# Performance work log

Hardware: AMD Instinct MI355X
Metric: run time of the kernel (lower is better)

Reference implementation:

```python
import jax, jax.numpy as jnp
import numpy as np

DN = ('NCHW', 'OIHW', 'NCHW')

def conv(x, w, b, stride=1, pad=1):
    y = jax.lax.conv_general_dilated(x, w, (stride, stride), [(pad, pad), (pad, pad)], dimension_numbers=DN)
    return y + b[None, :, None, None]

def conv_t(x, w, b):
    # torch ConvTranspose2d(k=4, s=2, p=1): implemented as lhs-dilated conv, pad = k-1-p = 2
    y = jax.lax.conv_general_dilated(x, w, (1, 1), [(2, 2), (2, 2)], lhs_dilation=(2, 2), dimension_numbers=DN)
    return y + b[None, :, None, None]

def residual_stack(x, rw3, rb3, rw1, rb1):
    # canonical VQ-VAE residual block: x + conv1x1(relu(conv3x3(relu(x)))), then final relu
    n = rw3.shape[0]
    for i in range(n):
        h = conv(jax.nn.relu(x), rw3[i], rb3[i], 1, 1)
        h = conv(jax.nn.relu(h), rw1[i], rb1[i], 1, 0)
        x = x + h
    return jax.nn.relu(x)

def vq(x, codebook, beta):
    # x: [N, D, H, W] -> [N, H, W, D]
    x = jnp.transpose(x, (0, 2, 3, 1))
    shp = x.shape
    xf = x.reshape(-1, shp[-1])                               # [T, D]
    d = (jnp.sum(xf * xf, 1, keepdims=True)
         + jnp.sum(codebook * codebook, 1)
         - 2.0 * xf @ codebook.T)                             # [T, K]
    idx = jnp.argmin(d, axis=1)                               # [T]
    enc = jax.nn.one_hot(idx, codebook.shape[0], dtype=x.dtype)
    q = jnp.take(codebook, idx, axis=0).reshape(shp)
    loss_e = jnp.mean((jax.lax.stop_gradient(q) - x) ** 2)
    loss_q = jnp.mean((q - jax.lax.stop_gradient(x)) ** 2)
    loss = loss_q + beta * loss_e
    q_st = x + jax.lax.stop_gradient(q - x)
    p = jnp.mean(enc, axis=0)
    perplexity = jnp.exp(-jnp.sum(p * jnp.log(p + 1e-10)))
    return loss, jnp.transpose(q_st, (0, 3, 1, 2)), perplexity, enc

def setup_inputs() -> dict:
    key = jax.random.key(0)
    ks = jax.random.split(key, 24)
    C_img, C, RH, NR, K, D = 3, 128, 32, 2, 512, 64
    def g(k, shape, fan_in):
        return jax.random.normal(k, shape, jnp.float32) * (1.0 / np.sqrt(fan_in))
    inp = {
        'x': jax.random.normal(ks[0], (16, C_img, 256, 256), jnp.float32),
        'enc_w1': g(ks[1], (C // 2, C_img, 4, 4), C_img * 16), 'enc_b1': jnp.zeros((C // 2,)),
        'enc_w2': g(ks[2], (C, C // 2, 4, 4), C // 2 * 16), 'enc_b2': jnp.zeros((C,)),
        'enc_w3': g(ks[3], (C, C, 3, 3), C * 9), 'enc_b3': jnp.zeros((C,)),
        'enc_rw3': g(ks[4], (NR, RH, C, 3, 3), C * 9), 'enc_rb3': jnp.zeros((NR, RH)),
        'enc_rw1': g(ks[5], (NR, C, RH, 1, 1), RH), 'enc_rb1': jnp.zeros((NR, C)),
        'pre_w': g(ks[6], (D, C, 1, 1), C), 'pre_b': jnp.zeros((D,)),
        'codebook': jax.random.uniform(ks[7], (K, D), jnp.float32, -1.0 / K, 1.0 / K),
        'dec_w1': g(ks[8], (C, D, 3, 3), D * 9), 'dec_b1': jnp.zeros((C,)),
        'dec_rw3': g(ks[9], (NR, RH, C, 3, 3), C * 9), 'dec_rb3': jnp.zeros((NR, RH)),
        'dec_rw1': g(ks[10], (NR, C, RH, 1, 1), RH), 'dec_rb1': jnp.zeros((NR, C)),
        'dec_dw1': g(ks[11], (C // 2, C, 4, 4), C * 16), 'dec_db1': jnp.zeros((C // 2,)),
        'dec_dw2': g(ks[12], (C_img, C // 2, 4, 4), C // 2 * 16), 'dec_db2': jnp.zeros((C_img,)),
    }
    return inp

def reference(x, enc_w1, enc_b1, enc_w2, enc_b2, enc_w3, enc_b3, enc_rw3, enc_rb3, enc_rw1, enc_rb1,
              pre_w, pre_b, codebook, dec_w1, dec_b1, dec_rw3, dec_rb3, dec_rw1, dec_rb1,
              dec_dw1, dec_db1, dec_dw2, dec_db2):
    beta = 0.25
    # encoder
    h = jax.nn.relu(conv(x, enc_w1, enc_b1, 2, 1))
    h = jax.nn.relu(conv(h, enc_w2, enc_b2, 2, 1))
    h = conv(h, enc_w3, enc_b3, 1, 1)
    h = residual_stack(h, enc_rw3, enc_rb3, enc_rw1, enc_rb1)
    # pre-VQ 1x1 conv
    z = conv(h, pre_w, pre_b, 1, 0)
    # vector quantization
    loss, q, perplexity, _ = vq(z, codebook, beta)
    # decoder
    d = conv(q, dec_w1, dec_b1, 1, 1)
    d = residual_stack(d, dec_rw3, dec_rb3, dec_rw1, dec_rb1)
    d = jax.nn.relu(conv_t(d, dec_dw1, dec_db1))
    x_recon = conv_t(d, dec_dw2, dec_db2)
    return loss, x_recon, perplexity
```

## Files before the change

### kernel.cpp

```cpp
#include <hip/hip_runtime.h>

typedef __attribute__((ext_vector_type(8)))  short bf16x8;
typedef __attribute__((ext_vector_type(16))) float f32x16;
typedef unsigned long long u64t;

__device__ __forceinline__ int swzu(int u)
{
    return u ^ (((u >> 3) & 1) | (((u >> 4) & 1) << 1));
}

__device__ __forceinline__ void fsplit(float v, unsigned short& h, unsigned short& l)
{
    union { float f; unsigned u; } a; a.f = v;
    unsigned uh = a.u + 0x7fffu + ((a.u >> 16) & 1u);
    h = (unsigned short)(uh >> 16);
    union { float f; unsigned u; } hb; hb.u = (unsigned)h << 16;
    float r = v - hb.f;
    union { float f; unsigned u; } b; b.f = r;
    unsigned ul = b.u + 0x7fffu + ((b.u >> 16) & 1u);
    l = (unsigned short)(ul >> 16);
}

__device__ __forceinline__ float bf2f(unsigned short u)
{
    union { float f; unsigned v; } a; a.v = (unsigned)u << 16; return a.f;
}

__global__ void pack_w(const float* __restrict__ w, unsigned short* __restrict__ hi,
                       unsigned short* __restrict__ lo, int Cout, int Cin, int KK,
                       int CoP, int CiP)
{
    int i = blockIdx.x * 256 + threadIdx.x;
    int tot = KK * CoP * CiP;
    if (i >= tot) return;
    int t  = i / (CoP * CiP);
    int r  = i - t * (CoP * CiP);
    int co = r / CiP;
    int ci = r - co * CiP;
    float v = (co < Cout && ci < Cin) ? w[((size_t)co * Cin + ci) * KK + t] : 0.f;
    unsigned short h, l;
    fsplit(v, h, l);
    hi[i] = h; lo[i] = l;
}

__global__ void cb_norm(const float* __restrict__ cb, float* __restrict__ cn)
{
    int i = blockIdx.x * 256 + threadIdx.x;
    if (i >= 512) return;
    float s = 0.f;
    for (int d = 0; d < 64; d++) s = fmaf(cb[i*64+d], cb[i*64+d], s);
    cn[i] = s;
}

__global__ __launch_bounds__(256) void pack_x(const float* __restrict__ x,
    unsigned short* __restrict__ PH)
{
    int idx = blockIdx.x * 256 + threadIdx.x;
    int n = idx >> 16, pix = idx & 65535;
    unsigned short h[8], l[8];
#pragma unroll
    for (int c = 0; c < 8; c++) h[c] = 0;
#pragma unroll
    for (int c = 0; c < 3; c++) {
        float v = x[((size_t)(n * 3 + c) << 16) + pix];
        fsplit(v, h[c], l[c]);
    }
    uint4 hv;
    hv.x = h[0] | ((unsigned)h[1] << 16); hv.y = h[2] | ((unsigned)h[3] << 16);
    hv.z = h[4] | ((unsigned)h[5] << 16); hv.w = h[6] | ((unsigned)h[7] << 16);
    uint4 z4 = make_uint4(0, 0, 0, 0);
    size_t b0 = (((size_t)(n * 2) << 16) + pix) * 8;
    size_t b1 = (((size_t)(n * 2 + 1) << 16) + pix) * 8;
    *(uint4*)(PH + b0) = hv;
    *(uint4*)(PH + b1) = z4;
}

template<int K,int S,int P,int CIP,int COUT,int HIN,int WIN,int HOUT,int WOUT,
         int TR,int TC,int WM,int WN,int PX2,int CO2,int CC,int CO_PAD,
         bool PACK,bool PRELU,bool PLO,bool WF32,bool ROUT,bool RES>
__global__ __launch_bounds__(256) void conv_mfma(
    const unsigned short* __restrict__ inH,
    const unsigned short* __restrict__ wpH,
    const float* __restrict__ bias, const float* __restrict__ res,
    float* __restrict__ outF, unsigned short* __restrict__ outPH,
    unsigned short* __restrict__ outPL)
{
    constexpr int IHT = (TR - 1) * S + K;
    constexpr int IW  = (TC - 1) * S + K;
    constexpr int PS  = IHT * IW;
    constexpr int PLN = CC * 2;
    constexpr int UN  = PS * PLN;
    constexpr int KK  = K * K;
    constexpr int NCH = CIP / (CC * 16);
    constexpr int NBUF = (NCH > 1) ? 2 : 1;
    constexpr int CG  = CIP / 8;
    constexpr int CGO = (COUT + 7) / 8;
    constexpr int XB  = WOUT / TC;
    constexpr int REGU = (UN + 255) / 256;
    constexpr int NST = CC * KK;

    __shared__ uint4 lbH[NBUF * UN];

    const int tid = threadIdx.x;
    const int bx  = blockIdx.x;
    const int r0  = (bx / XB) * TR;
    const int c0  = (bx % XB) * TC;
    const int co0 = blockIdx.y * (WM * CO2 * 32);
    const int n   = blockIdx.z;

    const int l  = tid & 63, wv = tid >> 6;
    const int wm = wv / WN, wn = wv % WN;
    const int ln = l & 31, kg = l >> 5;

    int pb[PX2], gyv[PX2], gxv[PX2];
#pragma unroll
    for (int p2 = 0; p2 < PX2; p2++) {
        int q = wn * (PX2 * 32) + p2 * 32 + ln;
        int lr = q / TC, lc = q % TC;
        pb[p2] = (lr * S) * IW + lc * S;
        gyv[p2] = r0 + lr; gxv[p2] = c0 + lc;
    }

    const int iy0 = r0 * S - P, ix0 = c0 * S - P;
    const size_t inb = (size_t)n * CG * HIN * WIN;

    f32x16 acc[PX2][CO2];
#pragma unroll
    for (int p2 = 0; p2 < PX2; p2++)
#pragma unroll
        for (int g = 0; g < CO2; g++) acc[p2][g] = (f32x16){};

    auto unit_load = [&](int u, int cgb, uint4& hv){
        int kgu = u / PS, pos = u - kgu * PS;
        int py = pos / IW, px = pos - py * IW;
        int gy = iy0 + py, gx = ix0 + px;
        bool ok = ((unsigned)gy < (unsigned)HIN) && ((unsigned)gx < (unsigned)WIN);
        hv = make_uint4(0,0,0,0);
        if (ok) {
            size_t a = (inb + ((size_t)(cgb + kgu) * HIN + gy) * WIN + gx) * 8;
            hv = *(const uint4*)(inH + a);
        }
    };

    auto stage_direct = [&](int kc, int b){
        for (int idx = tid; idx < UN; idx += 256) {
            uint4 hv;
            unit_load(idx, kc * PLN, hv);
            lbH[b * UN + swzu(idx)] = hv;
        }
    };

    uint4 rvH[REGU];
    auto load_regs = [&](int kc){
#pragma unroll
        for (int rr = 0; rr < REGU; rr++) {
            int idx = tid + rr * 256;
            uint4 hv = make_uint4(0,0,0,0);
            if (idx < UN) unit_load(idx, kc * PLN, hv);
            rvH[rr] = hv;
        }
    };
    auto write_regs = [&](int b){
#pragma unroll
        for (int rr = 0; rr < REGU; rr++) {
            int idx = tid + rr * 256;
            if (idx < UN) lbH[b * UN + swzu(idx)] = rvH[rr];
        }
    };

    auto compute = [&](int kc, int b){
        bf16x8 aR[3][CO2], bR[2][PX2];
        auto loadA = [&](int step, bf16x8 (&a)[CO2]){
            const int ks = step / KK, t = step - ks * KK;
#pragma unroll
            for (int g = 0; g < CO2; g++) {
                const int coA = co0 + (wm * CO2 + g) * 32 + ln;
                const size_t wo = ((size_t)t * CO_PAD + coA) * CIP
                                + kc * (CC * 16) + ks * 16 + kg * 8;
                a[g] = *(const bf16x8*)(wpH + wo);
            }
        };
        auto loadB = [&](int step, bf16x8 (&bv)[PX2]){
            const int ks = step / KK, t = step - ks * KK;
            const int ky = t / K, kx = t - ky * K;
#pragma unroll
            for (int p2 = 0; p2 < PX2; p2++) {
                const int u = (ks * 2 + kg) * PS + pb[p2] + ky * IW + kx;
                bv[p2] = *(const bf16x8*)&lbH[b * UN + swzu(u)];
            }
        };
        loadA(0, aR[0]);
        if (NST > 1) loadA(1, aR[1]);
        loadB(0, bR[0]);
#pragma unroll
        for (int step = 0; step < NST; step++) {
            if (step + 2 < NST) loadA(step + 2, aR[(step + 2) % 3]);
            if (step + 1 < NST) loadB(step + 1, bR[(step + 1) & 1]);
#pragma unroll
            for (int p2 = 0; p2 < PX2; p2++)
#pragma unroll
                for (int g = 0; g < CO2; g++)
                    acc[p2][g] = __builtin_amdgcn_mfma_f32_32x32x16_bf16(
                        aR[step % 3][g], bR[step & 1][p2], acc[p2][g], 0, 0, 0);
        }
    };

    stage_direct(0, 0);
    __syncthreads();
    int cur = 0;
    for (int kc = 0; kc < NCH; kc++) {
        const bool more = (kc + 1 < NCH);
        if (more) load_regs(kc + 1);
        compute(kc, cur);
        if (more) {
            write_regs(cur ^ 1);
            __syncthreads();
            cur ^= 1;
        }
    }

    const size_t HWo = (size_t)HOUT * WOUT;
#pragma unroll
    for (int p2 = 0; p2 < PX2; p2++) {
        const int gy = gyv[p2], gx = gxv[p2];
#pragma unroll
        for (int g = 0; g < CO2; g++) {
            const int co32 = co0 + (wm * CO2 + g) * 32;
#pragma unroll
            for (int rq = 0; rq < 4; rq++) {
                const int cb4 = co32 + 8 * rq + 4 * kg;
                float v[4];
#pragma unroll
                for (int i = 0; i < 4; i++) {
                    const int r = rq * 4 + i;
                    const int co = cb4 + i;
                    float bv = (co < COUT) ? bias[co] : 0.f;
                    float vv = acc[p2][g][r] + bv;
                    if (RES && co < COUT)
                        vv += res[((size_t)n * COUT + co) * HWo + (size_t)gy * WOUT + gx];
                    if (ROUT) vv = fmaxf(vv, 0.f);
                    if (WF32 && co < COUT)
                        outF[((size_t)n * COUT + co) * HWo + (size_t)gy * WOUT + gx] = vv;
                    v[i] = vv;
                }
                if (PACK) {
                    u64t uh = 0, ul = 0;
#pragma unroll
                    for (int i = 0; i < 4; i++) {
                        float pv = PRELU ? fmaxf(v[i], 0.f) : v[i];
                        unsigned short ph, pl;
                        fsplit(pv, ph, pl);
                        uh |= (u64t)ph << (16 * i);
                        ul |= (u64t)pl << (16 * i);
                    }
                    size_t pa = (((size_t)n * CGO + (co32 >> 3) + rq) * HOUT + gy) * (size_t)WOUT * 8
                              + (size_t)gx * 8 + 4 * kg;
                    *(u64t*)(outPH + pa) = uh;
                    if (PLO) *(u64t*)(outPL + pa) = ul;
                }
            }
// ... 41 lines not shown
        float v[4];
#pragma unroll
        for (int i = 0; i < 4; i++) {
            const int r = rq * 4 + i;
            const int co = cb4 + i;
            float bv = (co < COUT) ? bias[co] : 0.f;
            float vv = acc[r] + bv;
            if (RES && co < COUT)
                vv += res[((size_t)n * COUT + co) * HW + pix];
            if (ROUT) vv = fmaxf(vv, 0.f);
            if (WF32 && co < COUT)
                outF[((size_t)n * COUT + co) * HW + pix] = vv;
            v[i] = vv;
        }
        if (PACK) {
            u64t uh = 0, ul = 0;
#pragma unroll
            for (int i = 0; i < 4; i++) {
                float pv = PRELU ? fmaxf(v[i], 0.f) : v[i];
                unsigned short ph, pl;
                fsplit(pv, ph, pl);
                uh |= (u64t)ph << (16 * i);
                ul |= (u64t)pl << (16 * i);
            }
            size_t pa = (((size_t)n * CGO + (co32 >> 3) + rq) * HW + pix) * 8 + 4 * kg;
            *(u64t*)(outPH + pa) = uh;
            if (PLO) *(u64t*)(outPL + pa) = ul;
        }
    }
}

template<int CIP,int COUT,int HIN,int WIN,int CO2,int CC,int CO_PAD,
         bool PACK,bool WF32,bool ROUT>
__global__ __launch_bounds__(256) void convt_mfma(
    const unsigned short* __restrict__ inH,
    const unsigned short* __restrict__ wpH,
    const float* __restrict__ bias, float* __restrict__ outF,
    unsigned short* __restrict__ outPH)
{
    constexpr int HOUT = 2 * HIN, WOUT = 2 * WIN;
    constexpr int XHN  = WOUT / 128;
    constexpr int PS   = 3 * 68;
    constexpr int PLN  = CC * 2;
    constexpr int UN   = PS * PLN;
    constexpr int NCH  = CIP / (CC * 16);
    constexpr int NBUF = (NCH > 1) ? 2 : 1;
    constexpr int CG   = CIP / 8;
    constexpr int CGO  = (COUT + 7) / 8;
    constexpr int REGU = (UN + 255) / 256;
    constexpr int NST  = CC * 4;

    __shared__ uint4 lbH[NBUF * UN];

    const int tid = threadIdx.x;
    const int xh  = blockIdx.x % XHN;
    const int gr  = blockIdx.x / XHN;
    const int oy0 = (gr >> 1) * 4 + (gr & 1);
    const int co0 = blockIdx.y * (CO2 * 32);
    const int n   = blockIdx.z;

    const int ky0 = oy0 & 1;
    const int iyb = ((oy0 + ky0) >> 1) - 1;

    const int l  = tid & 63, wv = tid >> 6;
    const int pw = wv & 1, xb = wv >> 1;
    const int ln = l & 31, kg = l >> 5;

    const size_t inb = (size_t)n * CG * HIN * WIN;

    f32x16 acc[2][CO2];
#pragma unroll
    for (int r2 = 0; r2 < 2; r2++)
#pragma unroll
        for (int g = 0; g < CO2; g++) acc[r2][g] = (f32x16){};

    auto unit_load = [&](int u, int cgb, uint4& hv){
        int kgu = u / PS, pos = u - kgu * PS;
        int rr = pos / 68, cc = pos - rr * 68;
        int gy = iyb + rr, gx = xh * 64 + cc - 1;
        bool ok = ((unsigned)gy < (unsigned)HIN) && ((unsigned)gx < (unsigned)WIN);
        hv = make_uint4(0,0,0,0);
        if (ok) {
            size_t a = (inb + ((size_t)(cgb + kgu) * HIN + gy) * WIN + gx) * 8;
            hv = *(const uint4*)(inH + a);
        }
    };

    auto stage_direct = [&](int kc, int b){
        for (int idx = tid; idx < UN; idx += 256) {
            uint4 hv;
            unit_load(idx, kc * PLN, hv);
            lbH[b * UN + swzu(idx)] = hv;
        }
    };

    uint4 rvH[REGU];
    auto load_regs = [&](int kc){
#pragma unroll
        for (int rr = 0; rr < REGU; rr++) {
            int idx = tid + rr * 256;
            uint4 hv = make_uint4(0,0,0,0);
            if (idx < UN) unit_load(idx, kc * PLN, hv);
            rvH[rr] = hv;
        }
    };
    auto write_regs = [&](int b){
#pragma unroll
        for (int rr = 0; rr < REGU; rr++) {
            int idx = tid + rr * 256;
            if (idx < UN) lbH[b * UN + swzu(idx)] = rvH[rr];
        }
    };

    auto compute = [&](int kc, int b){
        bf16x8 aR[3][CO2], bR[2][2];
        auto loadA = [&](int step, bf16x8 (&a)[CO2]){
            const int ks = step / 4, tt = step - ks * 4;
            const int widx = (ky0 + 2 * (tt >> 1)) * 4 + (pw + 2 * (tt & 1));
#pragma unroll
            for (int g = 0; g < CO2; g++) {
                const int coA = co0 + g * 32 + ln;
                const size_t wo = ((size_t)widx * CO_PAD + coA) * CIP
                                + kc * (CC * 16) + ks * 16 + kg * 8;
                a[g] = *(const bf16x8*)(wpH + wo);
            }
        };
        auto loadB = [&](int step, bf16x8 (&bv)[2]){
            const int ks = step / 4, tt = step - ks * 4;
            const int ty = tt >> 1, tx = tt & 1;
#pragma unroll
            for (int r2 = 0; r2 < 2; r2++) {
                const int u = (ks * 2 + kg) * PS + (r2 + ty) * 68 + xb * 32 + ln + pw + tx;
                bv[r2] = *(const bf16x8*)&lbH[b * UN + swzu(u)];
            }
        };
        loadA(0, aR[0]);
        if (NST > 1) loadA(1, aR[1]);
        loadB(0, bR[0]);
#pragma unroll
        for (int step = 0; step < NST; step++) {
            if (step + 2 < NST) loadA(step + 2, aR[(step + 2) % 3]);
            if (step + 1 < NST) loadB(step + 1, bR[(step + 1) & 1]);
#pragma unroll
            for (int r2 = 0; r2 < 2; r2++)
#pragma unroll
                for (int g = 0; g < CO2; g++)
                    acc[r2][g] = __builtin_amdgcn_mfma_f32_32x32x16_bf16(
                        aR[step % 3][g], bR[step & 1][r2], acc[r2][g], 0, 0, 0);
        }
    };

    stage_direct(0, 0);
    __syncthreads();
    int cur = 0;
    for (int kc = 0; kc < NCH; kc++) {
        const bool more = (kc + 1 < NCH);
        if (more) load_regs(kc + 1);
        compute(kc, cur);
        if (more) {
            write_regs(cur ^ 1);
            __syncthreads();
            cur ^= 1;
        }
    }

    const int ox = xh * 128 + pw + 2 * (xb * 32 + ln);
    const size_t HWo = (size_t)HOUT * WOUT;
#pragma unroll
    for (int r2 = 0; r2 < 2; r2++) {
        const int oy = oy0 + 2 * r2;
#pragma unroll
        for (int g = 0; g < CO2; g++) {
            const int co32 = co0 + g * 32;
#pragma unroll
            for (int rq = 0; rq < 4; rq++) {
                const int cb4 = co32 + 8 * rq + 4 * kg;
                float v[4];
#pragma unroll
                for (int i = 0; i < 4; i++) {
                    const int r = rq * 4 + i;
                    const int co = cb4 + i;
                    float bv = (co < COUT) ? bias[co] : 0.f;
                    float vv = acc[r2][g][r] + bv;
                    if (ROUT) vv = fmaxf(vv, 0.f);
                    if (WF32 && co < COUT)
                        outF[((size_t)n * COUT + co) * HWo + (size_t)oy * WOUT + ox] = vv;
                    v[i] = vv;
                }
                if (PACK) {
                    u64t uh = 0;
#pragma unroll
                    for (int i = 0; i < 4; i++) {
                        unsigned short ph, pl;
                        fsplit(v[i], ph, pl);
                        uh |= (u64t)ph << (16 * i);
                    }
                    size_t pa = (((size_t)n * CGO + (co32 >> 3) + rq) * HOUT + oy) * (size_t)WOUT * 8
                              + (size_t)ox * 8 + 4 * kg;
                    *(u64t*)(outPH + pa) = uh;
                }
            }
        }
    }
}

__global__ __launch_bounds__(256) void vq_mfma(
    const unsigned short* __restrict__ zPH, const unsigned short* __restrict__ zPL,
    const unsigned short* __restrict__ cbH, const unsigned short* __restrict__ cbL,
    const float* __restrict__ cnorm,
    unsigned short* __restrict__ qPH,
    float* __restrict__ ssep, int* __restrict__ hist)
{
    __shared__ unsigned short zH[128 * 72];
    __shared__ unsigned short zL[128 * 72];
    __shared__ float cnl[512];
    __shared__ int   hl[512];

    const int tid = threadIdx.x;
    const int blk = blockIdx.x;

    for (int i = tid; i < 512; i += 256) { cnl[i] = cnorm[i]; hl[i] = 0; }

    for (int idx = tid; idx < 1024; idx += 256) {
        int tok = idx >> 3, cg = idx & 7;
        int t = blk * 128 + tok;
        int n = t >> 12, pix = t & 4095;
        size_t a = (((size_t)(n * 8 + cg)) * 4096 + pix) * 8;
        *(uint4*)&zH[tok * 72 + cg * 8] = *(const uint4*)(zPH + a);
        *(uint4*)&zL[tok * 72 + cg * 8] = *(const uint4*)(zPL + a);
    }
    __syncthreads();

    const int l  = tid & 63, wv = tid >> 6;
// ... 30 lines not shown
        for (int r = 0; r < 16; r++) {
            int m    = (r & 3) + 8 * (r >> 2) + 4 * kg;
            int code = cg * 32 + m;
            float s  = a0[r] + a1[r];
            float dm = cnl[code] - 2.f * s;
            if (dm < bm) { bm = dm; bidx = code; }
        }
    }

    float bm2 = __shfl_xor(bm, 32);
    int   bi2 = __shfl_xor(bidx, 32);
    if (bm2 < bm || (bm2 == bm && bi2 < bidx)) { bm = bm2; bidx = bi2; }

    {
        int t = blk * 128 + tok;
        int n = t >> 12, pix = t & 4095;
#pragma unroll
        for (int cgl = 0; cgl < 4; cgl++) {
            int cg = kg * 4 + cgl;
            uint4 hv = *(const uint4*)(cbH + (size_t)bidx * 64 + cg * 8);
            size_t a = (((size_t)(n * 8 + cg)) * 4096 + pix) * 8;
            *(uint4*)(qPH + a) = hv;
        }
    }

    float bestd = xn + bm;
    float c = (kg == 0) ? bestd : 0.f;
#pragma unroll
    for (int o = 32; o > 0; o >>= 1) c += __shfl_down(c, o, 64);
    if (l == 0) ssep[blk * 4 + wv] = c;
    if (kg == 0) atomicAdd(&hl[bidx], 1);
    __syncthreads();
    for (int i = tid; i < 512; i += 256) if (hl[i] > 0) atomicAdd(&hist[i], hl[i]);
}

__global__ void vq_init(int* hist)
{
    for (int i = threadIdx.x; i < 512; i += 256) hist[i] = 0;
}

__global__ __launch_bounds__(256) void vq_finalize(
    const float* __restrict__ ssep, const int* __restrict__ hist,
    float* __restrict__ o_loss, float* __restrict__ o_perp)
{
    __shared__ float red[256];
    const int tid = threadIdx.x;
    float h = 0.f;
    for (int i = tid; i < 512; i += 256) {
        float p = (float)hist[i] * (1.0f / 65536.0f);
        h -= p * logf(p + 1e-10f);
    }
    red[tid] = h;
    __syncthreads();
    for (int st = 128; st > 0; st >>= 1) {
        if (tid < st) red[tid] += red[tid + st];
        __syncthreads();
    }
    const float H = red[0];
    __syncthreads();
    float s = 0.f;
    for (int i = tid; i < 2048; i += 256) s += ssep[i];
    red[tid] = s;
    __syncthreads();
    for (int st = 128; st > 0; st >>= 1) {
        if (tid < st) red[tid] += red[tid + st];
        __syncthreads();
    }
    if (tid == 0) {
        *o_loss = 1.25f * red[0] / 4194304.0f;
        *o_perp = expf(H);
    }
// ... 26 lines not shown
    const float* dw1     = (const float*)d_in[20];
    const float* db1     = (const float*)d_in[21];
    const float* dw2     = (const float*)d_in[22];
    const float* db2     = (const float*)d_in[23];

    float* o      = (float*)d_out;
    float* loss_p = o;
    float* recon  = o + 1;
    float* perp_p = o + 1 + 16 * 3 * 256 * 256;

    unsigned short* R1H = (unsigned short*)d_ws;
    unsigned short* R1L = R1H + 16777216;
    unsigned short* R2H = R1L + 16777216;
    unsigned short* R2L = R2H + 16777216;
    float* Cf  = (float*)(R2L + 16777216);
    float* SSE = Cf + 8388608;
    int*   HIST = (int*)(SSE + 2048);

    unsigned short *xPH = R1H;
    unsigned short *BPH = R1H;
    unsigned short *zPH = R1H + 8388608, *zPL = R1L + 8388608;
    unsigned short *DtPH = R1H + 12582912;
    unsigned short *dAPH = R1H;
    unsigned short *APH = R2H;
    unsigned short *CPH = R2H;
    unsigned short *qPH = R2H + 8388608;

    unsigned short* wp_cur = (unsigned short*)(((size_t)(HIST + 512) + 31) & ~(size_t)31);
    auto carve = [&](size_t n_us) {
        unsigned short* p = wp_cur;
        wp_cur += ((n_us + 15) & ~(size_t)15);
        return p;
    };
    auto PK = [&](const float* w, unsigned short* hi, unsigned short* lo,
                  int Co, int Ci, int KK, int CoP, int CiP) {
        int tot = KK * CoP * CiP;
        pack_w<<<dim3((tot + 255) / 256), dim3(256), 0, stream>>>(w, hi, lo, Co, Ci, KK, CoP, CiP);
    };

    unsigned short *e1H = carve(16*64*16),  *e1L = carve(16*64*16);
    unsigned short *e2H = carve(16*128*64), *e2L = carve(16*128*64);
    unsigned short *e3H = carve(9*128*128), *e3L = carve(9*128*128);
    unsigned short *er3aH = carve(9*32*128), *er3aL = carve(9*32*128);
    unsigned short *er3bH = carve(9*32*128), *er3bL = carve(9*32*128);
    unsigned short *er1aH = carve(128*32),   *er1aL = carve(128*32);
    unsigned short *er1bH = carve(128*32),   *er1bL = carve(128*32);
    unsigned short *preH = carve(64*128),    *preL = carve(64*128);
    unsigned short *d1H  = carve(9*128*64),  *d1L  = carve(9*128*64);
    unsigned short *dr3aH = carve(9*32*128), *dr3aL = carve(9*32*128);
    unsigned short *dr3bH = carve(9*32*128), *dr3bL = carve(9*32*128);
    unsigned short *dr1aH = carve(128*32),   *dr1aL = carve(128*32);
    unsigned short *dr1bH = carve(128*32),   *dr1bL = carve(128*32);
    unsigned short *ct1H = carve(16*64*128), *ct1L = carve(16*64*128);
    unsigned short *ct2H = carve(16*32*64),  *ct2L = carve(16*32*64);
    unsigned short *cbH  = carve(512*64),    *cbL  = carve(512*64);
    float* CN = (float*)carve(1024);

    PK(enc_w1, e1H, e1L, 64, 3, 16, 64, 16);
    PK(enc_w2, e2H, e2L, 128, 64, 16, 128, 64);
    PK(enc_w3, e3H, e3L, 128, 128, 9, 128, 128);
    PK(enc_rw3,             er3aH, er3aL, 32, 128, 9, 32, 128);
    PK(enc_rw3 + 32*128*9,  er3bH, er3bL, 32, 128, 9, 32, 128);
    PK(enc_rw1,             er1aH, er1aL, 128, 32, 1, 128, 32);
    PK(enc_rw1 + 128*32,    er1bH, er1bL, 128, 32, 1, 128, 32);
    PK(pre_w, preH, preL, 64, 128, 1, 64, 128);
    PK(dec_w1, d1H, d1L, 128, 64, 9, 128, 64);
    PK(dec_rw3,             dr3aH, dr3aL, 32, 128, 9, 32, 128);
    PK(dec_rw3 + 32*128*9,  dr3bH, dr3bL, 32, 128, 9, 32, 128);
    PK(dec_rw1,             dr1aH, dr1aL, 128, 32, 1, 128, 32);
    PK(dec_rw1 + 128*32,    dr1bH, dr1bL, 128, 32, 1, 128, 32);
    PK(dw1, ct1H, ct1L, 64, 128, 16, 64, 128);
    PK(dw2, ct2H, ct2L, 3, 64, 16, 32, 64);
    PK(cb,  cbH,  cbL,  512, 64, 1, 512, 64);
    cb_norm<<<dim3(2), dim3(256), 0, stream>>>(cb, CN);
    pack_x<<<dim3(4096), dim3(256), 0, stream>>>(x, xPH);

    const int N = 16;

    conv_mfma<4,2,1, 16,64, 256,256, 128,128, 1,64, 2,2,1,1, 1, 64,
              true,false,false,false,true,false>
        <<<dim3(256,1,N),256,0,stream>>>(xPH, e1H, enc_b1, nullptr, nullptr, APH, nullptr);
    conv_mfma<4,2,1, 64,128, 128,128, 64,64, 1,64, 4,1,2,1, 1, 128,
              true,false,false,false,true,false>
        <<<dim3(64,1,N),256,0,stream>>>(APH, e2H, enc_b2, nullptr, nullptr, BPH, nullptr);
    conv_mfma<3,1,1, 128,128, 64,64, 64,64, 1,64, 4,1,2,1, 2, 128,
              true,true,false,true,false,false>
        <<<dim3(64,1,N),256,0,stream>>>(BPH, e3H, enc_b3, nullptr, Cf, CPH, nullptr);
    conv_mfma<3,1,1, 128,32, 64,64, 64,64, 2,64, 1,4,1,1, 4, 32,
              true,true,false,false,false,false>
        <<<dim3(32,1,N),256,0,stream>>>(CPH, er3aH, enc_rb3, nullptr, nullptr, DtPH, nullptr);
    conv1x1_mfma<32,128, 4096, 128,  true,true,false,true,false,true>
        <<<dim3(64,2,N),256,0,stream>>>(DtPH, er1aH, enc_rb1, Cf, Cf, CPH, nullptr);
    conv_mfma<3,1,1, 128,32, 64,64, 64,64, 2,64, 1,4,1,1, 4, 32,
              true,true,false,false,false,false>
        <<<dim3(32,1,N),256,0,stream>>>(CPH, er3bH, enc_rb3 + 32, nullptr, nullptr, DtPH, nullptr);
    conv1x1_mfma<32,128, 4096, 128,  true,true,false,true,false,true>
        <<<dim3(64,2,N),256,0,stream>>>(DtPH, er1bH, enc_rb1 + 128, Cf, Cf, CPH, nullptr);
    conv1x1_mfma<128,64, 4096, 64,   true,false,true,false,false,false>
        <<<dim3(64,1,N),256,0,stream>>>(CPH, preH, pre_b, nullptr, nullptr, zPH, zPL);

    vq_init<<<dim3(1), dim3(256), 0, stream>>>(HIST);
    vq_mfma<<<dim3(512), dim3(256), 0, stream>>>(zPH, zPL, cbH, cbL, CN, qPH, SSE, HIST);
    vq_finalize<<<dim3(1), dim3(256), 0, stream>>>(SSE, HIST, loss_p, perp_p);

    conv_mfma<3,1,1, 64,128, 64,64, 64,64, 1,64, 4,1,2,1, 2, 128,
              true,true,false,true,false,false>
        <<<dim3(64,1,N),256,0,stream>>>(qPH, d1H, dec_b1, nullptr, Cf, CPH, nullptr);
    conv_mfma<3,1,1, 128,32, 64,64, 64,64, 2,64, 1,4,1,1, 4, 32,
              true,true,false,false,false,false>
        <<<dim3(32,1,N),256,0,stream>>>(CPH, dr3aH, dec_rb3, nullptr, nullptr, DtPH, nullptr);
    conv1x1_mfma<32,128, 4096, 128,  true,true,false,true,false,true>
        <<<dim3(64,2,N),256,0,stream>>>(DtPH, dr1aH, dec_rb1, Cf, Cf, CPH, nullptr);
    conv_mfma<3,1,1, 128,32, 64,64, 64,64, 2,64, 1,4,1,1, 4, 32,
              true,true,false,false,false,false>
        <<<dim3(32,1,N),256,0,stream>>>(CPH, dr3bH, dec_rb3 + 32, nullptr, nullptr, DtPH, nullptr);
    conv1x1_mfma<32,128, 4096, 128,  true,true,false,true,false,true>
        <<<dim3(64,2,N),256,0,stream>>>(DtPH, dr1bH, dec_rb1 + 128, Cf, Cf, CPH, nullptr);
    convt_mfma<128,64, 64,64, 2, 2, 64,  true,false,true>
        <<<dim3(64,1,N),256,0,stream>>>(CPH, ct1H, db1, nullptr, dAPH);
    convt_mfma<64,3, 128,128, 1, 2, 32,  false,true,false>
        <<<dim3(256,1,N),256,0,stream>>>(dAPH, ct2H, db2, recon, nullptr);
}
```

Baseline: 552.7 us.

## Drop LDS staging in conv kernels; load operands directly from global memory

Replaces the shared-memory tiled conv and transposed-conv kernels with versions in which each wave reads its input pixels and weights straight from global memory into registers, using a 4-deep software prefetch pipeline and no barriers. Grids and per-wave tiling change to match: one wave per 32-pixel group, with output channels split across grid y. It also merges the sixteen weight-pack launches into one descriptor-driven kernel and folds histogram zeroing into the codebook-norm kernel, which cuts launch count. The trade-off is that neighbouring-tap reuse now relies on the L1/L2 caches instead of LDS, so global load traffic and latency exposure rise.

New measurement: 614.9 us. 11.3% more time.

```diff
diff --git a/kernel.cpp b/kernel.cpp
--- a/kernel.cpp
+++ b/kernel.cpp
@@ -3,11 +3,6 @@
 typedef __attribute__((ext_vector_type(8)))  short bf16x8;
 typedef __attribute__((ext_vector_type(16))) float f32x16;
 typedef unsigned long long u64t;
-
-__device__ __forceinline__ int swzu(int u)
-{
-    return u ^ (((u >> 3) & 1) | (((u >> 4) & 1) << 1));
-}
 
 __device__ __forceinline__ void fsplit(float v, unsigned short& h, unsigned short& l)
 {
@@ -26,30 +21,45 @@
     union { float f; unsigned v; } a; a.v = (unsigned)u << 16; return a.f;
 }
 
-__global__ void pack_w(const float* __restrict__ w, unsigned short* __restrict__ hi,
-                       unsigned short* __restrict__ lo, int Cout, int Cin, int KK,
-                       int CoP, int CiP)
-{
-    int i = blockIdx.x * 256 + threadIdx.x;
-    int tot = KK * CoP * CiP;
+struct PackDesc {
+    const float* w;
+    unsigned short *hi, *lo;
+    int Co, Ci, KK, CoP, CiP;
+    int blk0;
+};
+struct PackAll { PackDesc d[16]; int nd; };
+
+__global__ __launch_bounds__(256) void pack_all(PackAll pa)
+{
+    int bx = blockIdx.x;
+    int di = 0;
+#pragma unroll
+    for (int i = 0; i < 16; i++)
+        if (i < pa.nd && bx >= pa.d[i].blk0) di = i;
+    const PackDesc& D = pa.d[di];
+    int i = (bx - D.blk0) * 256 + threadIdx.x;
+    int tot = D.KK * D.CoP * D.CiP;
     if (i >= tot) return;
-    int t  = i / (CoP * CiP);
-    int r  = i - t * (CoP * CiP);
-    int co = r / CiP;
-    int ci = r - co * CiP;
-    float v = (co < Cout && ci < Cin) ? w[((size_t)co * Cin + ci) * KK + t] : 0.f;
+    int t  = i / (D.CoP * D.CiP);
+    int r  = i - t * (D.CoP * D.CiP);
+    int co = r / D.CiP;
+    int ci = r - co * D.CiP;
+    float v = (co < D.Co && ci < D.Ci) ? D.w[((size_t)co * D.Ci + ci) * D.KK + t] : 0.f;
     unsigned short h, l;
     fsplit(v, h, l);
-    hi[i] = h; lo[i] = l;
-}
-
-__global__ void cb_norm(const float* __restrict__ cb, float* __restrict__ cn)
+    D.hi[i] = h; D.lo[i] = l;
+}
+
+__global__ __launch_bounds__(256) void vq_prep(const float* __restrict__ cb,
+                                               float* __restrict__ cn, int* __restrict__ hist)
 {
     int i = blockIdx.x * 256 + threadIdx.x;
-    if (i >= 512) return;
-    float s = 0.f;
-    for (int d = 0; d < 64; d++) s = fmaf(cb[i*64+d], cb[i*64+d], s);
-    cn[i] = s;
+    if (i < 512) {
+        hist[i] = 0;
+        float s = 0.f;
+        for (int d = 0; d < 64; d++) s = fmaf(cb[i*64+d], cb[i*64+d], s);
+        cn[i] = s;
+    }
 }
 
 __global__ __launch_bounds__(256) void pack_x(const float* __restrict__ x,
@@ -76,52 +86,38 @@
 }
 
 template<int K,int S,int P,int CIP,int COUT,int HIN,int WIN,int HOUT,int WOUT,
-         int TR,int TC,int WM,int WN,int PX2,int CO2,int CC,int CO_PAD,
+         int PX2,int CO2,int CC,int CO_PAD,
          bool PACK,bool PRELU,bool PLO,bool WF32,bool ROUT,bool RES>
-__global__ __launch_bounds__(256) void conv_mfma(
+__global__ __launch_bounds__(256) void conv_nolds(
     const unsigned short* __restrict__ inH,
     const unsigned short* __restrict__ wpH,
     const float* __restrict__ bias, const float* __restrict__ res,
     float* __restrict__ outF, unsigned short* __restrict__ outPH,
     unsigned short* __restrict__ outPL)
 {
-    constexpr int IHT = (TR - 1) * S + K;
-    constexpr int IW  = (TC - 1) * S + K;
-    constexpr int PS  = IHT * IW;
-    constexpr int PLN = CC * 2;
-    constexpr int UN  = PS * PLN;
     constexpr int KK  = K * K;
     constexpr int NCH = CIP / (CC * 16);
-    constexpr int NBUF = (NCH > 1) ? 2 : 1;
+    constexpr int NST = CC * KK;
+    constexpr int TOT = NCH * NST;
     constexpr int CG  = CIP / 8;
     constexpr int CGO = (COUT + 7) / 8;
-    constexpr int XB  = WOUT / TC;
-    constexpr int REGU = (UN + 255) / 256;
-    constexpr int NST = CC * KK;
-
-    __shared__ uint4 lbH[NBUF * UN];
+    constexpr int PXB = 4 * PX2 * 32;
+    constexpr int LA  = (TOT < 3) ? (TOT - 1) : 3;
 
     const int tid = threadIdx.x;
-    const int bx  = blockIdx.x;
-    const int r0  = (bx / XB) * TR;
-    const int c0  = (bx % XB) * TC;
-    const int co0 = blockIdx.y * (WM * CO2 * 32);
+    const int l  = tid & 63, wv = tid >> 6;
+    const int ln = l & 31, kg = l >> 5;
+    const int co0 = blockIdx.y * (CO2 * 32);
     const int n   = blockIdx.z;
 
-    const int l  = tid & 63, wv = tid >> 6;
-    const int wm = wv / WN, wn = wv % WN;
-    const int ln = l & 31, kg = l >> 5;
-
-    int pb[PX2], gyv[PX2], gxv[PX2];
+    int gyv[PX2], gxv[PX2], iyb[PX2], ixb[PX2];
 #pragma unroll
     for (int p2 = 0; p2 < PX2; p2++) {
-        int q = wn * (PX2 * 32) + p2 * 32 + ln;
-        int lr = q / TC, lc = q % TC;
-        pb[p2] = (lr * S) * IW + lc * S;
-        gyv[p2] = r0 + lr; gxv[p2] = c0 + lc;
-    }
-
-    const int iy0 = r0 * S - P, ix0 = c0 * S - P;
+        int pix = blockIdx.x * PXB + wv * (PX2 * 32) + p2 * 32 + ln;
+        gyv[p2] = pix / WOUT; gxv[p2] = pix % WOUT;
+        iyb[p2] = gyv[p2] * S - P; ixb[p2] = gxv[p2] * S - P;
+    }
+
     const size_t inb = (size_t)n * CG * HIN * WIN;
 
     f32x16 acc[PX2][CO2];
@@ -130,93 +126,43 @@
 #pragma unroll
         for (int g = 0; g < CO2; g++) acc[p2][g] = (f32x16){};
 
-    auto unit_load = [&](int u, int cgb, uint4& hv){
-        int kgu = u / PS, pos = u - kgu * PS;
-        int py = pos / IW, px = pos - py * IW;
-        int gy = iy0 + py, gx = ix0 + px;
-        bool ok = ((unsigned)gy < (unsigned)HIN) && ((unsigned)gx < (unsigned)WIN);
-        hv = make_uint4(0,0,0,0);
-        if (ok) {
-            size_t a = (inb + ((size_t)(cgb + kgu) * HIN + gy) * WIN + gx) * 8;
-            hv = *(const uint4*)(inH + a);
+    auto loadA = [&](int gs, bf16x8 (&a)[CO2]){
+        const int kc = gs / NST, s = gs - kc * NST;
+        const int ks = s / KK, t = s - ks * KK;
+#pragma unroll
+        for (int g = 0; g < CO2; g++) {
+            const int coA = co0 + g * 32 + ln;
+            a[g] = *(const bf16x8*)(wpH + ((size_t)t * CO_PAD + coA) * CIP
+                                    + kc * (CC * 16) + ks * 16 + kg * 8);
         }
     };
-
-    auto stage_direct = [&](int kc, int b){
-        for (int idx = tid; idx < UN; idx += 256) {
-            uint4 hv;
-            unit_load(idx, kc * PLN, hv);
-            lbH[b * UN + swzu(idx)] = hv;
+    auto loadB = [&](int gs, bf16x8 (&b)[PX2]){
+        const int kc = gs / NST, s = gs - kc * NST;
+        const int ks = s / KK, t = s - ks * KK;
+        const int ky = t / K, kx = t - ky * K;
+        const int cg = kc * (CC * 2) + ks * 2 + kg;
+#pragma unroll
+        for (int p2 = 0; p2 < PX2; p2++) {
+            const int iy = iyb[p2] + ky, ix = ixb[p2] + kx;
+            bf16x8 v = {};
+            if ((unsigned)iy < (unsigned)HIN && (unsigned)ix < (unsigned)WIN)
+                v = *(const bf16x8*)(inH + (inb + ((size_t)cg * HIN + iy) * WIN + ix) * 8);
+            b[p2] = v;
         }
     };
 
-    uint4 rvH[REGU];
-    auto load_regs = [&](int kc){
-#pragma unroll
-        for (int rr = 0; rr < REGU; rr++) {
-            int idx = tid + rr * 256;
-            uint4 hv = make_uint4(0,0,0,0);
-            if (idx < UN) unit_load(idx, kc * PLN, hv);
-            rvH[rr] = hv;
-        }
-    };
-    auto write_regs = [&](int b){
-#pragma unroll
-        for (int rr = 0; rr < REGU; rr++) {
-            int idx = tid + rr * 256;
-            if (idx < UN) lbH[b * UN + swzu(idx)] = rvH[rr];
-        }
-    };
-
-    auto compute = [&](int kc, int b){
-        bf16x8 aR[3][CO2], bR[2][PX2];
-        auto loadA = [&](int step, bf16x8 (&a)[CO2]){
-            const int ks = step / KK, t = step - ks * KK;
-#pragma unroll
-            for (int g = 0; g < CO2; g++) {
-                const int coA = co0 + (wm * CO2 + g) * 32 + ln;
-                const size_t wo = ((size_t)t * CO_PAD + coA) * CIP
-                                + kc * (CC * 16) + ks * 16 + kg * 8;
-                a[g] = *(const bf16x8*)(wpH + wo);
-            }
-        };
-        auto loadB = [&](int step, bf16x8 (&bv)[PX2]){
-            const int ks = step / KK, t = step - ks * KK;
-            const int ky = t / K, kx = t - ky * K;
-#pragma unroll
-            for (int p2 = 0; p2 < PX2; p2++) {
-                const int u = (ks * 2 + kg) * PS + pb[p2] + ky * IW + kx;
-                bv[p2] = *(const bf16x8*)&lbH[b * UN + swzu(u)];
-            }
-        };
-        loadA(0, aR[0]);
-        if (NST > 1) loadA(1, aR[1]);
-        loadB(0, bR[0]);
-#pragma unroll
-        for (int step = 0; step < NST; step++) {
-            if (step + 2 < NST) loadA(step + 2, aR[(step + 2) % 3]);
-            if (step + 1 < NST) loadB(step + 1, bR[(step + 1) & 1]);
-#pragma unroll
-            for (int p2 = 0; p2 < PX2; p2++)
-#pragma unroll
-                for (int g = 0; g < CO2; g++)
-                    acc[p2][g] = __builtin_amdgcn_mfma_f32_32x32x16_bf16(
-                        aR[step % 3][g], bR[step & 1][p2], acc[p2][g], 0, 0, 0);
-        }
-    };
-
-    stage_direct(0, 0);
-    __syncthreads();
-    int cur = 0;
-    for (int kc = 0; kc < NCH; kc++) {
-        const bool more = (kc + 1 < NCH);
-        if (more) load_regs(kc + 1);
-        compute(kc, cur);
-        if (more) {
-            write_regs(cur ^ 1);
-            __syncthreads();
-            cur ^= 1;
-        }
+    bf16x8 aR[4][CO2], bR[4][PX2];
+#pragma unroll
+    for (int i = 0; i < LA; i++) { loadA(i, aR[i]); loadB(i, bR[i]); }
+#pragma unroll
+    for (int s = 0; s < TOT; s++) {
+        if (s + LA < TOT) { loadA(s + LA, aR[(s + LA) & 3]); loadB(s + LA, bR[(s + LA) & 3]); }
+#pragma unroll
+        for (int p2 = 0; p2 < PX2; p2++)
+#pragma unroll
+            for (int g = 0; g < CO2; g++)
+                acc[p2][g] = __builtin_amdgcn_mfma_f32_32x32x16_bf16(
+                    aR[s & 3][g], bR[s & 3][p2], acc[p2][g], 0, 0, 0);
     }
 
     const size_t HWo = (size_t)HOUT * WOUT;
@@ -225,7 +171,7 @@
         const int gy = gyv[p2], gx = gxv[p2];
 #pragma unroll
         for (int g = 0; g < CO2; g++) {
-            const int co32 = co0 + (wm * CO2 + g) * 32;
+            const int co32 = co0 + g * 32;
 #pragma unroll
             for (int rq = 0; rq < 4; rq++) {
                 const int cb4 = co32 + 8 * rq + 4 * kg;
@@ -333,7 +279,7 @@
 
 template<int CIP,int COUT,int HIN,int WIN,int CO2,int CC,int CO_PAD,
          bool PACK,bool WF32,bool ROUT>
-__global__ __launch_bounds__(256) void convt_mfma(
+__global__ __launch_bounds__(256) void convt_nolds(
     const unsigned short* __restrict__ inH,
     const unsigned short* __restrict__ wpH,
     const float* __restrict__ bias, float* __restrict__ outF,
@@ -341,165 +287,99 @@
 {
     constexpr int HOUT = 2 * HIN, WOUT = 2 * WIN;
     constexpr int XHN  = WOUT / 128;
-    constexpr int PS   = 3 * 68;
-    constexpr int PLN  = CC * 2;
-    constexpr int UN   = PS * PLN;
     constexpr int NCH  = CIP / (CC * 16);
-    constexpr int NBUF = (NCH > 1) ? 2 : 1;
+    constexpr int NST  = CC * 4;
+    constexpr int TOT  = NCH * NST;
     constexpr int CG   = CIP / 8;
     constexpr int CGO  = (COUT + 7) / 8;
-    constexpr int REGU = (UN + 255) / 256;
-    constexpr int NST  = CC * 4;
-
-    __shared__ uint4 lbH[NBUF * UN];
+    constexpr int LA   = (TOT < 3) ? (TOT - 1) : 3;
 
     const int tid = threadIdx.x;
+    const int oy  = blockIdx.x / XHN;
     const int xh  = blockIdx.x % XHN;
-    const int gr  = blockIdx.x / XHN;
-    const int oy0 = (gr >> 1) * 4 + (gr & 1);
     const int co0 = blockIdx.y * (CO2 * 32);
     const int n   = blockIdx.z;
 
-    const int ky0 = oy0 & 1;
-    const int iyb = ((oy0 + ky0) >> 1) - 1;
+    const int ky0 = oy & 1;
+    const int iyb = ((oy + ky0) >> 1) - 1;
 
     const int l  = tid & 63, wv = tid >> 6;
     const int pw = wv & 1, xb = wv >> 1;
     const int ln = l & 31, kg = l >> 5;
 
+    const int ixb = xh * 64 + xb * 32 + ln + pw - 1;
     const size_t inb = (size_t)n * CG * HIN * WIN;
 
-    f32x16 acc[2][CO2];
-#pragma unroll
-    for (int r2 = 0; r2 < 2; r2++)
-#pragma unroll
-        for (int g = 0; g < CO2; g++) acc[r2][g] = (f32x16){};
-
-    auto unit_load = [&](int u, int cgb, uint4& hv){
-        int kgu = u / PS, pos = u - kgu * PS;
-        int rr = pos / 68, cc = pos - rr * 68;
-        int gy = iyb + rr, gx = xh * 64 + cc - 1;
-        bool ok = ((unsigned)gy < (unsigned)HIN) && ((unsigned)gx < (unsigned)WIN);
-        hv = make_uint4(0,0,0,0);
-        if (ok) {
-            size_t a = (inb + ((size_t)(cgb + kgu) * HIN + gy) * WIN + gx) * 8;
-            hv = *(const uint4*)(inH + a);
+    f32x16 acc[CO2];
+#pragma unroll
+    for (int g = 0; g < CO2; g++) acc[g] = (f32x16){};
+
+    auto loadA = [&](int gs, bf16x8 (&a)[CO2]){
+        const int kc = gs / NST, s = gs - kc * NST;
+        const int ks = s / 4, tt = s - ks * 4;
+        const int widx = (ky0 + 2 * (tt >> 1)) * 4 + (pw + 2 * (tt & 1));
+#pragma unroll
+        for (int g = 0; g < CO2; g++) {
+            const int coA = co0 + g * 32 + ln;
+            a[g] = *(const bf16x8*)(wpH + ((size_t)widx * CO_PAD + coA) * CIP
+                                    + kc * (CC * 16) + ks * 16 + kg * 8);
         }
     };
-
-    auto stage_direct = [&](int kc, int b){
-        for (int idx = tid; idx < UN; idx += 256) {
-            uint4 hv;
-            unit_load(idx, kc * PLN, hv);
-            lbH[b * UN + swzu(idx)] = hv;
-        }
+    auto loadB = [&](int gs, bf16x8& b){
+        const int kc = gs / NST, s = gs - kc * NST;
+        const int ks = s / 4, tt = s - ks * 4;
+        const int ty = tt >> 1, tx = tt & 1;
+        const int cg = kc * (CC * 2) + ks * 2 + kg;
+        const int iy = iyb + ty, ix = ixb + tx;
+        bf16x8 v = {};
+        if ((unsigned)iy < (unsigned)HIN && (unsigned)ix < (unsigned)WIN)
+            v = *(const bf16x8*)(inH + (inb + ((size_t)cg * HIN + iy) * WIN + ix) * 8);
+        b = v;
     };
 
-    uint4 rvH[REGU];
-    auto load_regs = [&](int kc){
-#pragma unroll
-        for (int rr = 0; rr < REGU; rr++) {
-            int idx = tid + rr * 256;
-            uint4 hv = make_uint4(0,0,0,0);
-            if (idx < UN) unit_load(idx, kc * PLN, hv);
-            rvH[rr] = hv;
-        }
-    };
-    auto write_regs = [&](int b){
-#pragma unroll
-        for (int rr = 0; rr < REGU; rr++) {
-            int idx = tid + rr * 256;
-            if (idx < UN) lbH[b * UN + swzu(idx)] = rvH[rr];
-        }
-    };
-
-    auto compute = [&](int kc, int b){
-        bf16x8 aR[3][CO2], bR[2][2];
-        auto loadA = [&](int step, bf16x8 (&a)[CO2]){
-            const int ks = step / 4, tt = step - ks * 4;
-            const int widx = (ky0 + 2 * (tt >> 1)) * 4 + (pw + 2 * (tt & 1));
-#pragma unroll
-            for (int g = 0; g < CO2; g++) {
-                const int coA = co0 + g * 32 + ln;
-                const size_t wo = ((size_t)widx * CO_PAD + coA) * CIP
-                                + kc * (CC * 16) + ks * 16 + kg * 8;
-                a[g] = *(const bf16x8*)(wpH + wo);
-            }
-        };
-        auto loadB = [&](int step, bf16x8 (&bv)[2]){
-            const int ks = step / 4, tt = step - ks * 4;
-            const int ty = tt >> 1, tx = tt & 1;
-#pragma unroll
-            for (int r2 = 0; r2 < 2; r2++) {
-                const int u = (ks * 2 + kg) * PS + (r2 + ty) * 68 + xb * 32 + ln + pw + tx;
-                bv[r2] = *(const bf16x8*)&lbH[b * UN + swzu(u)];
-            }
-        };
-        loadA(0, aR[0]);
-        if (NST > 1) loadA(1, aR[1]);
-        loadB(0, bR[0]);
-#pragma unroll
-        for (int step = 0; step < NST; step++) {
-            if (step + 2 < NST) loadA(step + 2, aR[(step + 2) % 3]);
-            if (step + 1 < NST) loadB(step + 1, bR[(step + 1) & 1]);
-#pragma unroll
-            for (int r2 = 0; r2 < 2; r2++)
-#pragma unroll
-                for (int g = 0; g < CO2; g++)
-                    acc[r2][g] = __builtin_amdgcn_mfma_f32_32x32x16_bf16(
-                        aR[step % 3][g], bR[step & 1][r2], acc[r2][g], 0, 0, 0);
-        }
-    };
-
-    stage_direct(0, 0);
-    __syncthreads();
-    int cur = 0;
-    for (int kc = 0; kc < NCH; kc++) {
-        const bool more = (kc + 1 < NCH);
-        if (more) load_regs(kc + 1);
-        compute(kc, cur);
-        if (more) {
-            write_regs(cur ^ 1);
-            __syncthreads();
-            cur ^= 1;
-        }
+    bf16x8 aR[4][CO2], bR[4];
+#pragma unroll
+    for (int i = 0; i < LA; i++) { loadA(i, aR[i]); loadB(i, bR[i]); }
+#pragma unroll
+    for (int s = 0; s < TOT; s++) {
+        if (s + LA < TOT) { loadA(s + LA, aR[(s + LA) & 3]); loadB(s + LA, bR[(s + LA) & 3]); }
+#pragma unroll
+        for (int g = 0; g < CO2; g++)
+            acc[g] = __builtin_amdgcn_mfma_f32_32x32x16_bf16(
+                aR[s & 3][g], bR[s & 3], acc[g], 0, 0, 0);
     }
 
     const int ox = xh * 128 + pw + 2 * (xb * 32 + ln);
     const size_t HWo = (size_t)HOUT * WOUT;
 #pragma unroll
-    for (int r2 = 0; r2 < 2; r2++) {
-        const int oy = oy0 + 2 * r2;
-#pragma unroll
-        for (int g = 0; g < CO2; g++) {
-            const int co32 = co0 + g * 32;
-#pragma unroll
-            for (int rq = 0; rq < 4; rq++) {
-                const int cb4 = co32 + 8 * rq + 4 * kg;
-                float v[4];
+    for (int g = 0; g < CO2; g++) {
+        const int co32 = co0 + g * 32;
+#pragma unroll
+        for (int rq = 0; rq < 4; rq++) {
+            const int cb4 = co32 + 8 * rq + 4 * kg;
+            float v[4];
+#pragma unroll
+            for (int i = 0; i < 4; i++) {
+                const int r = rq * 4 + i;
+                const int co = cb4 + i;
+                float bv = (co < COUT) ? bias[co] : 0.f;
+                float vv = acc[g][r] + bv;
+                if (ROUT) vv = fmaxf(vv, 0.f);
+                if (WF32 && co < COUT)
+                    outF[((size_t)n * COUT + co) * HWo + (size_t)oy * WOUT + ox] = vv;
+                v[i] = vv;
+            }
+            if (PACK) {
+                u64t uh = 0;
 #pragma unroll
                 for (int i = 0; i < 4; i++) {
-                    const int r = rq * 4 + i;
-                    const int co = cb4 + i;
-                    float bv = (co < COUT) ? bias[co] : 0.f;
-                    float vv = acc[r2][g][r] + bv;
-                    if (ROUT) vv = fmaxf(vv, 0.f);
-                    if (WF32 && co < COUT)
-                        outF[((size_t)n * COUT + co) * HWo + (size_t)oy * WOUT + ox] = vv;
-                    v[i] = vv;
+                    unsigned short ph, pl;
+                    fsplit(v[i], ph, pl);
+                    uh |= (u64t)ph << (16 * i);
                 }
-                if (PACK) {
-                    u64t uh = 0;
-#pragma unroll
-                    for (int i = 0; i < 4; i++) {
-                        unsigned short ph, pl;
-                        fsplit(v[i], ph, pl);
-                        uh |= (u64t)ph << (16 * i);
-                    }
-                    size_t pa = (((size_t)n * CGO + (co32 >> 3) + rq) * HOUT + oy) * (size_t)WOUT * 8
-                              + (size_t)ox * 8 + 4 * kg;
-                    *(u64t*)(outPH + pa) = uh;
-                }
+                size_t pa = (((size_t)n * CGO + (co32 >> 3) + rq) * HOUT + oy) * (size_t)WOUT * 8
+                          + (size_t)ox * 8 + 4 * kg;
+                *(u64t*)(outPH + pa) = uh;
             }
         }
     }
@@ -596,11 +476,6 @@
     if (kg == 0) atomicAdd(&hl[bidx], 1);
     __syncthreads();
     for (int i = tid; i < 512; i += 256) if (hl[i] > 0) atomicAdd(&hist[i], hl[i]);
-}
-
-__global__ void vq_init(int* hist)
-{
-    for (int i = threadIdx.x; i < 512; i += 256) hist[i] = 0;
 }
 
 __global__ __launch_bounds__(256) void vq_finalize(
@@ -693,11 +568,6 @@
         wp_cur += ((n_us + 15) & ~(size_t)15);
         return p;
     };
-    auto PK = [&](const float* w, unsigned short* hi, unsigned short* lo,
-                  int Co, int Ci, int KK, int CoP, int CiP) {
-        int tot = KK * CoP * CiP;
-        pack_w<<<dim3((tot + 255) / 256), dim3(256), 0, stream>>>(w, hi, lo, Co, Ci, KK, CoP, CiP);
-    };
 
     unsigned short *e1H = carve(16*64*16),  *e1L = carve(16*64*16);
     unsigned short *e2H = carve(16*128*64), *e2L = carve(16*128*64);
@@ -717,68 +587,75 @@
     unsigned short *cbH  = carve(512*64),    *cbL  = carve(512*64);
     float* CN = (float*)carve(1024);
 
-    PK(enc_w1, e1H, e1L, 64, 3, 16, 64, 16);
-    PK(enc_w2, e2H, e2L, 128, 64, 16, 128, 64);
-    PK(enc_w3, e3H, e3L, 128, 128, 9, 128, 128);
-    PK(enc_rw3,             er3aH, er3aL, 32, 128, 9, 32, 128);
-    PK(enc_rw3 + 32*128*9,  er3bH, er3bL, 32, 128, 9, 32, 128);
-    PK(enc_rw1,             er1aH, er1aL, 128, 32, 1, 128, 32);
-    PK(enc_rw1 + 128*32,    er1bH, er1bL, 128, 32, 1, 128, 32);
-    PK(pre_w, preH, preL, 64, 128, 1, 64, 128);
-    PK(dec_w1, d1H, d1L, 128, 64, 9, 128, 64);
-    PK(dec_rw3,             dr3aH, dr3aL, 32, 128, 9, 32, 128);
-    PK(dec_rw3 + 32*128*9,  dr3bH, dr3bL, 32, 128, 9, 32, 128);
-    PK(dec_rw1,             dr1aH, dr1aL, 128, 32, 1, 128, 32);
-    PK(dec_rw1 + 128*32,    dr1bH, dr1bL, 128, 32, 1, 128, 32);
-    PK(dw1, ct1H, ct1L, 64, 128, 16, 64, 128);
-    PK(dw2, ct2H, ct2L, 3, 64, 16, 32, 64);
-    PK(cb,  cbH,  cbL,  512, 64, 1, 512, 64);
-    cb_norm<<<dim3(2), dim3(256), 0, stream>>>(cb, CN);
+    PackAll pa; int nb = 0;
+    auto addPK = [&](int i, const float* w, unsigned short* hi, unsigned short* lo,
+                     int Co, int Ci, int KK, int CoP, int CiP) {
+        pa.d[i] = {w, hi, lo, Co, Ci, KK, CoP, CiP, nb};
+        nb += (KK * CoP * CiP + 255) / 256;
+    };
+    addPK(0,  enc_w1, e1H, e1L, 64, 3, 16, 64, 16);
+    addPK(1,  enc_w2, e2H, e2L, 128, 64, 16, 128, 64);
+    addPK(2,  enc_w3, e3H, e3L, 128, 128, 9, 128, 128);
+    addPK(3,  enc_rw3,            er3aH, er3aL, 32, 128, 9, 32, 128);
+    addPK(4,  enc_rw3 + 32*128*9, er3bH, er3bL, 32, 128, 9, 32, 128);
+    addPK(5,  enc_rw1,            er1aH, er1aL, 128, 32, 1, 128, 32);
+    addPK(6,  enc_rw1 + 128*32,   er1bH, er1bL, 128, 32, 1, 128, 32);
+    addPK(7,  pre_w, preH, preL, 64, 128, 1, 64, 128);
+    addPK(8,  dec_w1, d1H, d1L, 128, 64, 9, 128, 64);
+    addPK(9,  dec_rw3,            dr3aH, dr3aL, 32, 128, 9, 32, 128);
+    addPK(10, dec_rw3 + 32*128*9, dr3bH, dr3bL, 32, 128, 9, 32, 128);
+    addPK(11, dec_rw1,            dr1aH, dr1aL, 128, 32, 1, 128, 32);
+    addPK(12, dec_rw1 + 128*32,   dr1bH, dr1bL, 128, 32, 1, 128, 32);
+    addPK(13, dw1, ct1H, ct1L, 64, 128, 16, 64, 128);
+    addPK(14, dw2, ct2H, ct2L, 3, 64, 16, 32, 64);
+    addPK(15, cb,  cbH,  cbL,  512, 64, 1, 512, 64);
+    pa.nd = 16;
+    pack_all<<<dim3(nb), dim3(256), 0, stream>>>(pa);
+    vq_prep<<<dim3(2), dim3(256), 0, stream>>>(cb, CN, HIST);
     pack_x<<<dim3(4096), dim3(256), 0, stream>>>(x, xPH);
 
     const int N = 16;
 
-    conv_mfma<4,2,1, 16,64, 256,256, 128,128, 1,64, 2,2,1,1, 1, 64,
-              true,false,false,false,true,false>
-        <<<dim3(256,1,N),256,0,stream>>>(xPH, e1H, enc_b1, nullptr, nullptr, APH, nullptr);
-    conv_mfma<4,2,1, 64,128, 128,128, 64,64, 1,64, 4,1,2,1, 1, 128,
-              true,false,false,false,true,false>
-        <<<dim3(64,1,N),256,0,stream>>>(APH, e2H, enc_b2, nullptr, nullptr, BPH, nullptr);
-    conv_mfma<3,1,1, 128,128, 64,64, 64,64, 1,64, 4,1,2,1, 2, 128,
-              true,true,false,true,false,false>
-        <<<dim3(64,1,N),256,0,stream>>>(BPH, e3H, enc_b3, nullptr, Cf, CPH, nullptr);
-    conv_mfma<3,1,1, 128,32, 64,64, 64,64, 2,64, 1,4,1,1, 4, 32,
-              true,true,false,false,false,false>
+    conv_nolds<4,2,1, 16,64, 256,256, 128,128, 2,1,1, 64,
+               true,false,false,false,true,false>
+        <<<dim3(64,2,N),256,0,stream>>>(xPH, e1H, enc_b1, nullptr, nullptr, APH, nullptr);
+    conv_nolds<4,2,1, 64,128, 128,128, 64,64, 2,1,2, 128,
+               true,false,false,false,true,false>
+        <<<dim3(16,4,N),256,0,stream>>>(APH, e2H, enc_b2, nullptr, nullptr, BPH, nullptr);
+    conv_nolds<3,1,1, 128,128, 64,64, 64,64, 2,1,2, 128,
+               true,true,false,true,false,false>
+        <<<dim3(16,4,N),256,0,stream>>>(BPH, e3H, enc_b3, nullptr, Cf, CPH, nullptr);
+    conv_nolds<3,1,1, 128,32, 64,64, 64,64, 1,1,2, 32,
+               true,true,false,false,false,false>
         <<<dim3(32,1,N),256,0,stream>>>(CPH, er3aH, enc_rb3, nullptr, nullptr, DtPH, nullptr);
     conv1x1_mfma<32,128, 4096, 128,  true,true,false,true,false,true>
         <<<dim3(64,2,N),256,0,stream>>>(DtPH, er1aH, enc_rb1, Cf, Cf, CPH, nullptr);
-    conv_mfma<3,1,1, 128,32, 64,64, 64,64, 2,64, 1,4,1,1, 4, 32,
-              true,true,false,false,false,false>
+    conv_nolds<3,1,1, 128,32, 64,64, 64,64, 1,1,2, 32,
+               true,true,false,false,false,false>
         <<<dim3(32,1,N),256,0,stream>>>(CPH, er3bH, enc_rb3 + 32, nullptr, nullptr, DtPH, nullptr);
     conv1x1_mfma<32,128, 4096, 128,  true,true,false,true,false,true>
         <<<dim3(64,2,N),256,0,stream>>>(DtPH, er1bH, enc_rb1 + 128, Cf, Cf, CPH, nullptr);
     conv1x1_mfma<128,64, 4096, 64,   true,false,true,false,false,false>
         <<<dim3(64,1,N),256,0,stream>>>(CPH, preH, pre_b, nullptr, nullptr, zPH, zPL);
 
-    vq_init<<<dim3(1), dim3(256), 0, stream>>>(HIST);
     vq_mfma<<<dim3(512), dim3(256), 0, stream>>>(zPH, zPL, cbH, cbL, CN, qPH, SSE, HIST);
     vq_finalize<<<dim3(1), dim3(256), 0, stream>>>(SSE, HIST, loss_p, perp_p);
 
-    conv_mfma<3,1,1, 64,128, 64,64, 64,64, 1,64, 4,1,2,1, 2, 128,
-              true,true,false,true,false,false>
-        <<<dim3(64,1,N),256,0,stream>>>(qPH, d1H, dec_b1, nullptr, Cf, CPH, nullptr);
-    conv_mfma<3,1,1, 128,32, 64,64, 64,64, 2,64, 1,4,1,1, 4, 32,
-              true,true,false,false,false,false>
+    conv_nolds<3,1,1, 64,128, 64,64, 64,64, 2,1,2, 128,
+               true,true,false,true,false,false>
+        <<<dim3(16,4,N),256,0,stream>>>(qPH, d1H, dec_b1, nullptr, Cf, CPH, nullptr);
+    conv_nolds<3,1,1, 128,32, 64,64, 64,64, 1,1,2, 32,
+               true,true,false,false,false,false>
         <<<dim3(32,1,N),256,0,stream>>>(CPH, dr3aH, dec_rb3, nullptr, nullptr, DtPH, nullptr);
     conv1x1_mfma<32,128, 4096, 128,  true,true,false,true,false,true>
         <<<dim3(64,2,N),256,0,stream>>>(DtPH, dr1aH, dec_rb1, Cf, Cf, CPH, nullptr);
-    conv_mfma<3,1,1, 128,32, 64,64, 64,64, 2,64, 1,4,1,1, 4, 32,
-              true,true,false,false,false,false>
+    conv_nolds<3,1,1, 128,32, 64,64, 64,64, 1,1,2, 32,
+               true,true,false,false,false,false>
         <<<dim3(32,1,N),256,0,stream>>>(CPH, dr3bH, dec_rb3 + 32, nullptr, nullptr, DtPH, nullptr);
     conv1x1_mfma<32,128, 4096, 128,  true,true,false,true,false,true>
         <<<dim3(64,2,N),256,0,stream>>>(DtPH, dr1bH, dec_rb1 + 128, Cf, Cf, CPH, nullptr);
-    convt_mfma<128,64, 64,64, 2, 2, 64,  true,false,true>
-        <<<dim3(64,1,N),256,0,stream>>>(CPH, ct1H, db1, nullptr, dAPH);
-    convt_mfma<64,3, 128,128, 1, 2, 32,  false,true,false>
-        <<<dim3(256,1,N),256,0,stream>>>(dAPH, ct2H, db2, recon, nullptr);
-}
+    convt_nolds<128,64, 64,64, 2, 2, 64,  true,false,true>
+        <<<dim3(128,1,N),256,0,stream>>>(CPH, ct1H, db1, nullptr, dAPH);
+    convt_nolds<64,3, 128,128, 1, 2, 32,  false,true,false>
+        <<<dim3(512,1,N),256,0,stream>>>(dAPH, ct2H, db2, recon, nullptr);
+}
```
